# Optimization experiments

Measured on AMD Instinct MI355X. Metric: run time of the kernel, lower is better.

The kernel has to match this reference:

```python
import jax, jax.numpy as jnp
import numpy as np

N = 50000
E = 800000
IN = 128
H = 128
OUT = 64
L = 2
THETA = 1.0
SCALE = 2.0


def setup_inputs() -> dict:
    key = jax.random.key(0)
    ks = jax.random.split(key, 12)
    g = lambda k, s: (jax.random.normal(k, s, jnp.float32) * 0.05)
    return {
        "x": jax.random.normal(ks[0], (N, IN), jnp.float32),
        "edge_index": jax.random.randint(ks[1], (2, E), 0, N),
        "mlp_w1": g(ks[2], (IN, 512)), "mlp_b1": jnp.zeros((512,), jnp.float32),
        "mlp_w2": g(ks[3], (512, 64)), "mlp_b2": jnp.zeros((64,), jnp.float32),
        "mlp_w3": g(ks[4], (64, OUT)), "mlp_b3": jnp.zeros((OUT,), jnp.float32),
        "parsing": jnp.ones((L, OUT, OUT), jnp.float32) / SCALE,
        "lin0_w": g(ks[5], (IN, H)), "lin0_b": jnp.zeros((H,), jnp.float32),
        "lin1_w": g(ks[6], (H, OUT)), "lin1_b": jnp.zeros((OUT,), jnp.float32),
        "conv_w1": g(ks[7], (L, H, H)),
        "conv_w2": g(ks[8], (L, H, H)),
    }


def reference(x, edge_index, mlp_w1, mlp_b1, mlp_w2, mlp_b2, mlp_w3, mlp_b3,
              parsing, lin0_w, lin0_b, lin1_w, lin1_b, conv_w1, conv_w2):
    row, col = edge_index[0], edge_index[1]  # start, end

    # --- learn_soft_edge3 (algebraically exact reduction of outer-product + bmm + diag) ---
    h = jax.nn.relu(x @ mlp_w1 + mlp_b1)
    h = jax.nn.relu(h @ mlp_w2 + mlp_b2)
    logits = h @ mlp_w3 + mlp_b3                      # [N, OUT]
    P = jax.nn.relu(SCALE * parsing[0])               # [OUT, OUT]
    # diag(outer(start,end) @ P)[e,c] = start[e,c] * (end @ P)[e,c]
    ew = jnp.sum(logits[row] * (logits @ P)[col], axis=1)  # [E]
    mean = ew.mean()
    var = jnp.var(ew, ddof=1)                          # torch.var is unbiased
    ew = (ew - mean) * jnp.sqrt(jnp.float32(1e-4) / var) + 1.0

    # --- GCN2 stack ---
    x0 = jax.nn.relu(x @ lin0_w + lin0_b)              # [N, H]
    # gcn_norm with self loops (weight 1)
    loop = jnp.arange(N)
    r = jnp.concatenate([row, loop])
    c = jnp.concatenate([col, loop])
    w = jnp.concatenate([ew, jnp.ones((N,), ew.dtype)])
    deg = jax.ops.segment_sum(w, c, num_segments=N)
    dinv = jnp.where(deg > 0, jax.lax.rsqrt(jnp.where(deg > 0, deg, 1.0)), 0.0)
    norm = dinv[r] * w * dinv[c]                       # [E+N]

    hcur = x0
    alpha = 0.0
    for ln in range(L):
        agg = jax.ops.segment_sum(norm[:, None] * hcur[r], c, num_segments=N)  # [N, H]
        agg = agg * (1.0 - alpha)
        x0a = alpha * x0
        beta = float(np.log(THETA / (ln + 1) + 1.0))
        out = (1.0 - beta) * agg + beta * (agg @ conv_w1[ln]) \
            + (1.0 - beta) * x0a + beta * (x0a @ conv_w2[ln])
        hcur = jax.nn.relu(out)
    return hcur @ lin1_w + lin1_b                      # [N, OUT]
```

## Files before the change

kernel.cpp:

```cpp
#include <hip/hip_runtime.h>
#include <hip/hip_bf16.h>
#include <hip/hip_fp16.h>
#include <math.h>

#define NN 50000
#define NE 800000

typedef __attribute__((ext_vector_type(8))) short bf16x8;
typedef __attribute__((ext_vector_type(4))) float f32x4;

__device__ __forceinline__ short f2bf(float f){
  unsigned u = __float_as_uint(f);
  unsigned r = (u + 0x7fffu + ((u >> 16) & 1u)) >> 16;
  return (short)r;
}
__device__ __forceinline__ float bf2f(short s){
  return __uint_as_float(((unsigned)(unsigned short)s) << 16);
}

__device__ __forceinline__ unsigned f2fp8(float f){
  __half h = __float2half(f * 0.00390625f);
  unsigned hb = (unsigned)__half_as_ushort(h);
  unsigned s = hb >> 15;
  unsigned mag = hb & 0x7fffu;
  mag = mag + 0x3fu + ((mag >> 7) & 1u);
  unsigned m8 = mag >> 7;
  if (m8 > 0x7eu) m8 = 0x7eu;
  return (s << 7) | m8;
}
__device__ __forceinline__ void fp8x4_dec(unsigned u, float2& lo, float2& hi){
  unsigned l = ((u & 0x80u) << 8) | ((u & 0x7fu) << 7)
             | ((u & 0x8000u) << 16) | ((u & 0x7f00u) << 15);
  unsigned h = ((u & 0x800000u) >> 8) | ((u & 0x7f0000u) >> 9)
             | (u & 0x80000000u) | ((u & 0x7f000000u) >> 1);
  __half2 hl = *(__half2*)&l;
  __half2 hh = *(__half2*)&h;
  lo = __half22float2(hl);
  hi = __half22float2(hh);
}
__device__ __forceinline__ float fp8_dot4(unsigned a, unsigned b){
  float2 al, ah, bl, bh;
  fp8x4_dec(a, al, ah); fp8x4_dec(b, bl, bh);
  return al.x*bl.x + al.y*bl.y + ah.x*bh.x + ah.y*bh.y;
}

__global__ __launch_bounds__(256) void prep_k(const float* __restrict__ w1,
    const float* __restrict__ w2, const float* __restrict__ w3, const float* __restrict__ pars,
    const float* __restrict__ lin0w, const float* __restrict__ cw1, const float* __restrict__ lin1w,
    short* __restrict__ w1t, short* __restrict__ w2t, short* __restrict__ w3t, short* __restrict__ Pt,
    short* __restrict__ lin0wt, short* __restrict__ cw1t0, short* __restrict__ cw1t1,
    short* __restrict__ lin1wt, int* __restrict__ cnt, float* __restrict__ scal){
  int idx = blockIdx.x*256 + threadIdx.x;
  if (idx < NN) cnt[idx] = 0;
  if (idx < 16) scal[idx] = 0.0f;
  if (idx < 65536){
    int n = idx >> 7, k = idx & 127;
    w1t[idx] = f2bf(w1[k*512 + n]);
  } else if (idx < 98304){
    int i = idx - 65536; int n = i >> 9, k = i & 511;
    w2t[i] = f2bf(w2[k*64 + n]);
  } else if (idx < 102400){
    int i = idx - 98304; int n = i >> 6, k = i & 63;
    w3t[i] = f2bf(w3[k*64 + n]);
  } else if (idx < 106496){
    int i = idx - 102400; int n = i >> 6, k = i & 63;
    Pt[i] = f2bf(fmaxf(2.f*pars[k*64 + n], 0.f));
  } else if (idx < 122880){
    int i = idx - 106496; int n = i >> 7, k = i & 127;
    lin0wt[i] = f2bf(lin0w[k*128 + n]);
  } else if (idx < 139264){
    int i = idx - 122880; int n = i >> 7, k = i & 127;
    cw1t0[i] = f2bf(cw1[k*128 + n]);
  } else if (idx < 155648){
    int i = idx - 139264; int n = i >> 7, k = i & 127;
    cw1t1[i] = f2bf(cw1[16384 + k*128 + n]);
  } else if (idx < 163840){
    int i = idx - 155648; int n = i >> 7, k = i & 127;
    lin1wt[i] = f2bf(lin1w[k*64 + n]);
  }
}

__global__ __launch_bounds__(256) void mlp_mfma_k(
    const float* __restrict__ x,
    const short* __restrict__ w1t, const float* __restrict__ b1,
    const short* __restrict__ w2t, const float* __restrict__ b2,
    const short* __restrict__ w3t, const float* __restrict__ b3,
    const short* __restrict__ Pt,
    unsigned char* __restrict__ lg8, unsigned char* __restrict__ lgp8,
    short* __restrict__ xb, int M)
{
  __shared__ short xs [32][136];
  __shared__ short h1s[32][264];
  __shared__ short h2s[32][72];
  __shared__ short lgs[32][72];
  const int t = threadIdx.x;
  const int wave = t >> 6, lane = t & 63;
  const int quad = lane >> 4, l16 = lane & 15;
  const int m0 = blockIdx.x * 32;

  for (int task = t; task < 512; task += 256){
    int row = task >> 4, c0 = (task & 15) * 8;
    float4 v0 = make_float4(0,0,0,0), v1 = v0;
    int gm = m0 + row;
    if (gm < M){
      v0 = *(const float4*)(x + (size_t)gm*128 + c0);
      v1 = *(const float4*)(x + (size_t)gm*128 + c0 + 4);
    }
    bf16x8 s;
    s[0]=f2bf(v0.x); s[1]=f2bf(v0.y); s[2]=f2bf(v0.z); s[3]=f2bf(v0.w);
    s[4]=f2bf(v1.x); s[5]=f2bf(v1.y); s[6]=f2bf(v1.z); s[7]=f2bf(v1.w);
    *(bf16x8*)&xs[row][c0] = s;
    if (gm < M) *(bf16x8*)(xb + (size_t)gm*128 + c0) = s;
  }
  __syncthreads();

  f32x4 acc2[2];
  acc2[0] = (f32x4){0.f,0.f,0.f,0.f}; acc2[1] = acc2[0];
  const int n2 = wave*16 + l16;

  #pragma unroll
  for (int half = 0; half < 2; half++){
    {
      f32x4 acc[2][4];
      #pragma unroll
      for (int mt=0;mt<2;mt++)
        #pragma unroll
        for (int nt=0;nt<4;nt++) acc[mt][nt] = (f32x4){0.f,0.f,0.f,0.f};
      #pragma unroll
      for (int k0 = 0; k0 < 128; k0 += 32){
        bf16x8 a0 = *(const bf16x8*)&xs[l16     ][k0 + quad*8];
        bf16x8 a1 = *(const bf16x8*)&xs[16 + l16][k0 + quad*8];
        #pragma unroll
        for (int nt = 0; nt < 4; nt++){
          int n = half*256 + wave*64 + nt*16 + l16;
          bf16x8 b = *(const bf16x8*)(w1t + (size_t)n*128 + k0 + quad*8);
          acc[0][nt] = __builtin_amdgcn_mfma_f32_16x16x32_bf16(a0, b, acc[0][nt], 0,0,0);
          acc[1][nt] = __builtin_amdgcn_mfma_f32_16x16x32_bf16(a1, b, acc[1][nt], 0,0,0);
        }
      }
      #pragma unroll
      for (int nt = 0; nt < 4; nt++){
        int n  = half*256 + wave*64 + nt*16 + l16;
        int cl = wave*64 + nt*16 + l16;
        float bb = b1[n];
        #pragma unroll
        for (int mt = 0; mt < 2; mt++){
          #pragma unroll
          for (int r = 0; r < 4; r++){
            int row = mt*16 + quad*4 + r;
            h1s[row][cl] = f2bf(fmaxf(acc[mt][nt][r] + bb, 0.f));
          }
        }
      }
    }
    __syncthreads();

    for (int k0 = 0; k0 < 256; k0 += 32){
      bf16x8 b  = *(const bf16x8*)(w2t + (size_t)n2*512 + half*256 + k0 + quad*8);
      bf16x8 a0 = *(const bf16x8*)&h1s[l16     ][k0 + quad*8];
      bf16x8 a1 = *(const bf16x8*)&h1s[16 + l16][k0 + quad*8];
      acc2[0] = __builtin_amdgcn_mfma_f32_16x16x32_bf16(a0, b, acc2[0], 0,0,0);
      acc2[1] = __builtin_amdgcn_mfma_f32_16x16x32_bf16(a1, b, acc2[1], 0,0,0);
    }
    if (half == 0) __syncthreads();
  }

  {
    float bb = b2[n2];
    #pragma unroll
    for (int mt = 0; mt < 2; mt++)
      #pragma unroll
      for (int r = 0; r < 4; r++)
        h2s[mt*16 + quad*4 + r][n2] = f2bf(fmaxf(acc2[mt][r] + bb, 0.f));
  }
  __syncthreads();

  {
    f32x4 acc[2];
    acc[0] = (f32x4){0.f,0.f,0.f,0.f}; acc[1] = acc[0];
    for (int k0 = 0; k0 < 64; k0 += 32){
      bf16x8 b  = *(const bf16x8*)(w3t + (size_t)n2*64 + k0 + quad*8);
      bf16x8 a0 = *(const bf16x8*)&h2s[l16     ][k0 + quad*8];
      bf16x8 a1 = *(const bf16x8*)&h2s[16 + l16][k0 + quad*8];
      acc[0] = __builtin_amdgcn_mfma_f32_16x16x32_bf16(a0, b, acc[0], 0,0,0);
      acc[1] = __builtin_amdgcn_mfma_f32_16x16x32_bf16(a1, b, acc[1], 0,0,0);
    }
    float bb = b3[n2];
    #pragma unroll
    for (int mt = 0; mt < 2; mt++)
      #pragma unroll
      for (int r = 0; r < 4; r++)
        lgs[mt*16 + quad*4 + r][n2] = f2bf(acc[mt][r] + bb);
  }
  __syncthreads();

  {
    f32x4 acc[2];
    acc[0] = (f32x4){0.f,0.f,0.f,0.f}; acc[1] = acc[0];
    for (int k0 = 0; k0 < 64; k0 += 32){
      bf16x8 b  = *(const bf16x8*)(Pt + (size_t)n2*64 + k0 + quad*8);
      bf16x8 a0 = *(const bf16x8*)&lgs[l16     ][k0 + quad*8];
      bf16x8 a1 = *(const bf16x8*)&lgs[16 + l16][k0 + quad*8];
      acc[0] = __builtin_amdgcn_mfma_f32_16x16x32_bf16(a0, b, acc[0], 0,0,0);
      acc[1] = __builtin_amdgcn_mfma_f32_16x16x32_bf16(a1, b, acc[1], 0,0,0);
    }
    #pragma unroll
    for (int mt = 0; mt < 2; mt++)
      #pragma unroll
      for (int r = 0; r < 4; r++)
        h2s[mt*16 + quad*4 + r][n2] = f2bf(acc[mt][r]);
  }
  __syncthreads();

  {
    int row = t >> 3, c0 = (t & 7) * 8;
    int gm = m0 + row;
    if (gm < M){
      const short* pl = &lgs[row][c0];
      const short* pp = &h2s[row][c0];
      unsigned a0 = 0, a1 = 0, b0 = 0, b1 = 0;
      #pragma unroll
      for (int j = 0; j < 4; j++){
        a0 |= f2fp8(bf2f(pl[j]))     << (8*j);
        a1 |= f2fp8(bf2f(pl[4+j]))   << (8*j);
        b0 |= f2fp8(bf2f(pp[j]))     << (8*j);
        b1 |= f2fp8(bf2f(pp[4+j]))   << (8*j);
      }
      uint2 av; av.x = a0; av.y = a1;
      uint2 bv; bv.x = b0; bv.y = b1;
      *(uint2*)(lg8  + (size_t)gm*64 + c0) = av;
      *(uint2*)(lgp8 + (size_t)gm*64 + c0) = bv;
    }
  }
}

template<int NT, bool RELU, bool RESID, bool BF16OUT, bool SCALEROW>
__global__ __launch_bounds__(256) void bgemm_k(
    const short* __restrict__ A, const short* __restrict__ Bt,
    const float* __restrict__ bias, const short* __restrict__ extra,
    const float* __restrict__ dinvp,
    float* __restrict__ C, short* __restrict__ Cb, int M, float beta)
{
  const int N = NT*64;
  __shared__ short As[32][136];
  const int t = threadIdx.x;
  const int wave = t >> 6, lane = t & 63;
  const int quad = lane >> 4, l16 = lane & 15;
  const int m0 = blockIdx.x * 32;

  for (int task = t; task < 512; task += 256){
    int row = task >> 4, c0 = (task & 15) * 8;
    bf16x8 v = {0,0,0,0,0,0,0,0};
    if (m0 + row < M) v = *(const bf16x8*)(A + (size_t)(m0+row)*128 + c0);
    *(bf16x8*)&As[row][c0] = v;
  }
  __syncthreads();

  f32x4 acc[2][NT];
  #pragma unroll
  for (int mt=0;mt<2;mt++)
    #pragma unroll
    for (int nt=0;nt<NT;nt++) acc[mt][nt] = (f32x4){0.f,0.f,0.f,0.f};

  #pragma unroll
  for (int k0 = 0; k0 < 128; k0 += 32){
    bf16x8 a0 = *(const bf16x8*)&As[l16     ][k0 + quad*8];
    bf16x8 a1 = *(const bf16x8*)&As[16 + l16][k0 + quad*8];
    #pragma unroll
    for (int nt = 0; nt < NT; nt++){
      int n = (wave*NT + nt)*16 + l16;
      bf16x8 b = *(const bf16x8*)(Bt + (size_t)n*128 + k0 + quad*8);
      acc[0][nt] = __builtin_amdgcn_mfma_f32_16x16x32_bf16(a0, b, acc[0][nt], 0,0,0);
      acc[1][nt] = __builtin_amdgcn_mfma_f32_16x16x32_bf16(a1, b, acc[1][nt], 0,0,0);
    }
  }

  #pragma unroll
  for (int nt = 0; nt < NT; nt++){
    int n = (wave*NT + nt)*16 + l16;
    float bb = (bias != nullptr) ? bias[n] : 0.f;
    #pragma unroll
    for (int mt = 0; mt < 2; mt++){
      #pragma unroll
      for (int r = 0; r < 4; r++){
        int gm = m0 + mt*16 + quad*4 + r;
        if (gm >= M) continue;
        float v = acc[mt][nt][r];
        if (RESID){
          float ex = bf2f(extra[(size_t)gm*N + n]);
          v = beta*v + (1.f - beta)*ex;
        }
        v += bb;
        if (RELU) v = fmaxf(v, 0.f);
        if (SCALEROW) v *= dinvp[gm];
        if (BF16OUT) Cb[(size_t)gm*N + n] = f2bf(v);
        else         C [(size_t)gm*N + n] = v;
      }
    }
  }
}

__global__ __launch_bounds__(256) void count_k(const int* __restrict__ col, int* __restrict__ cnt,
    int* __restrict__ rank, int E){
  int i = (blockIdx.x*256 + threadIdx.x)*4;
  if (i + 3 < E){
    int4 c = *(const int4*)(col + i);
    int r0 = atomicAdd(&cnt[c.x], 1);
    int r1 = atomicAdd(&cnt[c.y], 1);
    int r2 = atomicAdd(&cnt[c.z], 1);
    int r3 = atomicAdd(&cnt[c.w], 1);
    *(int4*)(rank + i) = make_int4(r0, r1, r2, r3);
  } else {
    for (; i < E; i++) rank[i] = atomicAdd(&cnt[col[i]], 1);
  }
}

__global__ __launch_bounds__(256) void scan_sums_k(const int* __restrict__ cnt, int* __restrict__ bsum, int n){
  __shared__ int s[256];
  const int t = threadIdx.x;
  int i = blockIdx.x*1024 + t*4;
  int4 v = make_int4(0,0,0,0);
  if (i + 3 < n) v = *(const int4*)(cnt + i);
  else {
    if (i   < n) v.x = cnt[i];
    if (i+1 < n) v.y = cnt[i+1];
    if (i+2 < n) v.z = cnt[i+2];
    if (i+3 < n) v.w = cnt[i+3];
  }
  s[t] = v.x + v.y + v.z + v.w;
  __syncthreads();
  for (int st = 128; st; st >>= 1){
    if (t < st) s[t] += s[t + st];
    __syncthreads();
  }
  if (t == 0) bsum[blockIdx.x] = s[0];
}

__global__ __launch_bounds__(256) void scan_final_k(const int* __restrict__ cnt, const int* __restrict__ bsum,
    int* __restrict__ off, int n, int total, int nb){
  __shared__ int s[256];
  __shared__ int basebs;
  const int t = threadIdx.x;
  if (t < 64){
    int v = (t < nb && t < (int)blockIdx.x) ? bsum[t] : 0;
    #pragma unroll
    for (int o = 1; o < 64; o <<= 1) v += __shfl_xor(v, o);
    if (t == 0) basebs = v;
  }
  int i = blockIdx.x*1024 + t*4;
  int4 v = make_int4(0,0,0,0);
  if (i + 3 < n) v = *(const int4*)(cnt + i);
  else {
    if (i   < n) v.x = cnt[i];
    if (i+1 < n) v.y = cnt[i+1];
    if (i+2 < n) v.z = cnt[i+2];
    if (i+3 < n) v.w = cnt[i+3];
  }
  int tsum = v.x + v.y + v.z + v.w;
  s[t] = tsum;
  __syncthreads();
  #pragma unroll
  for (int st = 1; st < 256; st <<= 1){
    int a = (t >= st) ? s[t - st] : 0;
    __syncthreads();
    s[t] += a;
    __syncthreads();
  }
  int base = s[t] - tsum + basebs;
  int o0 = base, o1 = o0 + v.x, o2 = o1 + v.y, o3 = o2 + v.z;
  if (i   < n) off[i]   = o0;
  if (i+1 < n) off[i+1] = o1;
  if (i+2 < n) off[i+2] = o2;
  if (i+3 < n) off[i+3] = o3;
  if (blockIdx.x == 0 && t == 0) off[n] = total;
}

__global__ __launch_bounds__(256) void scatter_k(const int* __restrict__ row, const int* __restrict__ col,
    const int* __restrict__ off, const int* __restrict__ rank,
    int2* __restrict__ csr_sd, int E){
  int i = (blockIdx.x*256 + threadIdx.x)*4;
  if (i + 3 < E){
    int4 r = *(const int4*)(row + i);
    int4 c = *(const int4*)(col + i);
    int4 k = *(const int4*)(rank + i);
    int o0 = off[c.x], o1 = off[c.y], o2 = off[c.z], o3 = off[c.w];
    int2 p0; p0.x = r.x; p0.y = c.x;
    int2 p1; p1.x = r.y; p1.y = c.y;
    int2 p2; p2.x = r.z; p2.y = c.z;
    int2 p3; p3.x = r.w; p3.y = c.w;
    csr_sd[o0 + k.x] = p0;
    csr_sd[o1 + k.y] = p1;
    csr_sd[o2 + k.z] = p2;
    csr_sd[o3 + k.w] = p3;
  } else {
    for (; i < E; i++){
      int2 p; p.x = row[i]; p.y = col[i];
      csr_sd[off[col[i]] + rank[i]] = p;
    }
  }
}

__global__ __launch_bounds__(256) void ew2_k(const unsigned char* __restrict__ lg8,
    const unsigned char* __restrict__ lgp8,
    const int2* __restrict__ sd,
    float* __restrict__ w, float* __restrict__ scal, int E){
  const int t = threadIdx.x;
  const int lane = t & 63, wid = t >> 6;
  const int g = lane >> 4, q = lane & 15;
  const int gid = (blockIdx.x*4 + wid)*4 + g;
  const int ngroups = gridDim.x*16;
  float s = 0.f, ss = 0.f;
  for (int base = gid*4; base < E; base += ngroups*4){
    int4 p01 = *(const int4*)(sd + base);
    int4 p23 = *(const int4*)(sd + base + 2);
    unsigned a0 = *(const unsigned*)(lg8  + (size_t)p01.x*64 + q*4);
    unsigned a1 = *(const unsigned*)(lg8  + (size_t)p01.z*64 + q*4);
    unsigned a2 = *(const unsigned*)(lg8  + (size_t)p23.x*64 + q*4);
    unsigned a3 = *(const unsigned*)(lg8  + (size_t)p23.z*64 + q*4);
    unsigned b0 = *(const unsigned*)(lgp8 + (size_t)p01.y*64 + q*4);
    unsigned b1 = *(const unsigned*)(lgp8 + (size_t)p01.w*64 + q*4);
    unsigned b2 = *(const unsigned*)(lgp8 + (size_t)p23.y*64 + q*4);
    unsigned b3 = *(const unsigned*)(lgp8 + (size_t)p23.w*64 + q*4);
    float v0 = fp8_dot4(a0, b0);
    float v1 = fp8_dot4(a1, b1);
    float v2 = fp8_dot4(a2, b2);
    float v3 = fp8_dot4(a3, b3);
    #pragma unroll
    for (int o = 1; o < 16; o <<= 1){
      v0 += __shfl_xor(v0, o); v1 += __shfl_xor(v1, o);
      v2 += __shfl_xor(v2, o); v3 += __shfl_xor(v3, o);
    }
    if (q == 0){
      float4 vv = make_float4(v0*65536.f, v1*65536.f, v2*65536.f, v3*65536.f);
      *(float4*)(w + base) = vv;
      s  += vv.x + vv.y + vv.z + vv.w;
      ss += vv.x*vv.x + vv.y*vv.y + vv.z*vv.z + vv.w*vv.w;
    }
  }
  #pragma unroll
  for (int o = 1; o < 64; o <<= 1){ s += __shfl_xor(s, o); ss += __shfl_xor(ss, o); }
  __shared__ float ls[4], lss[4];
  if (lane == 0){ ls[wid] = s; lss[wid] = ss; }
  __syncthreads();
  if (t == 0){
    atomicAdd(&scal[0], ls[0]+ls[1]+ls[2]+ls[3]);
    atomicAdd(&scal[1], lss[0]+lss[1]+lss[2]+lss[3]);
  }
}

__global__ __launch_bounds__(256) void degnorm_k(float* __restrict__ w, const int* __restrict__ off,
    const float* __restrict__ scal, float* __restrict__ dinv, int Nn, int E){
  int n = blockIdx.x*256 + threadIdx.x;
  if (n < Nn){
    double sum = (double)scal[0], sumsq = (double)scal[1];
    double mean_d = sum / (double)E;
    double var    = (sumsq - sum*sum/(double)E) / (double)(E-1);
    float mean = (float)mean_d;
    float k    = (float)sqrt(1e-4 / var);
    int s = off[n], e = off[n+1];
    float d = 1.0f;
    for (int j = s; j < e; j++){
      float v = (w[j] - mean) * k + 1.0f;
      w[j] = v;
      d += v;
    }
    dinv[n] = (d > 0.f) ? rsqrtf(d) : 0.f;
  }
}

__global__ __launch_bounds__(256) void agg_gather_k(const short* __restrict__ hb,
    const int* __restrict__ off, const int2* __restrict__ sd, const float* __restrict__ w,
    const float* __restrict__ dinv, short* __restrict__ aggb, int Nn){
  int n = blockIdx.x*4 + (threadIdx.x >> 6);
  int lane = threadIdx.x & 63;
  if (n >= Nn) return;
  float d = dinv[n];
  short2 hv = *(const short2*)(hb + (size_t)n*128 + lane*2);
  float acc0 = bf2f(hv.x), acc1 = bf2f(hv.y);
  int s = off[n], e = off[n+1];
  int j = s;
  for (; j + 7 < e; j += 8){
    int4 p0 = *(const int4*)(sd + j);
    int4 p1 = *(const int4*)(sd + j + 2);
    int4 p2 = *(const int4*)(sd + j + 4);
    int4 p3 = *(const int4*)(sd + j + 6);
    float4 w0 = *(const float4*)(w + j);
    float4 w1 = *(const float4*)(w + j + 4);
    short2 h0 = *(const short2*)(hb + (size_t)p0.x*128 + lane*2);
    short2 h1 = *(const short2*)(hb + (size_t)p0.z*128 + lane*2);
    short2 h2 = *(const short2*)(hb + (size_t)p1.x*128 + lane*2);
    short2 h3 = *(const short2*)(hb + (size_t)p1.z*128 + lane*2);
    short2 h4 = *(const short2*)(hb + (size_t)p2.x*128 + lane*2);
    short2 h5 = *(const short2*)(hb + (size_t)p2.z*128 + lane*2);
    short2 h6 = *(const short2*)(hb + (size_t)p3.x*128 + lane*2);
    short2 h7 = *(const short2*)(hb + (size_t)p3.z*128 + lane*2);
    acc0 += w0.x*bf2f(h0.x) + w0.y*bf2f(h1.x) + w0.z*bf2f(h2.x) + w0.w*bf2f(h3.x)
          + w1.x*bf2f(h4.x) + w1.y*bf2f(h5.x) + w1.z*bf2f(h6.x) + w1.w*bf2f(h7.x);
    acc1 += w0.x*bf2f(h0.y) + w0.y*bf2f(h1.y) + w0.z*bf2f(h2.y) + w0.w*bf2f(h3.y)
          + w1.x*bf2f(h4.y) + w1.y*bf2f(h5.y) + w1.z*bf2f(h6.y) + w1.w*bf2f(h7.y);
  }
  for (; j < e; j++){
    int2 p = sd[j];
    short2 h0 = *(const short2*)(hb + (size_t)p.x*128 + lane*2);
    float w0 = w[j];
    acc0 += w0*bf2f(h0.x); acc1 += w0*bf2f(h0.y);
  }
  acc0 *= d; acc1 *= d;
  short2 o; o.x = f2bf(acc0); o.y = f2bf(acc1);
  *(short2*)(aggb + (size_t)n*128 + lane*2) = o;
}

extern "C" void kernel_launch(void* const* d_in, const int* in_sizes, int n_in,
                              void* d_out, int out_size, void* d_ws, size_t ws_size,
                              hipStream_t stream){
  const float* x      = (const float*)d_in[0];
  const int*   ei     = (const int*)  d_in[1];
  const float* w1     = (const float*)d_in[2];
  const float* b1     = (const float*)d_in[3];
  const float* w2     = (const float*)d_in[4];
  const float* b2     = (const float*)d_in[5];
  const float* w3     = (const float*)d_in[6];
  const float* b3     = (const float*)d_in[7];
  const float* pars   = (const float*)d_in[8];
  const float* lin0w  = (const float*)d_in[9];
  const float* lin0b  = (const float*)d_in[10];
  const float* lin1w  = (const float*)d_in[11];
  const float* lin1b  = (const float*)d_in[12];
  const float* cw1    = (const float*)d_in[13];
  float* out          = (float*)d_out;

  float* ws = (float*)d_ws;
  int*   cnt     = (int*)(ws + 0);
  int*   off     = (int*)(ws + 50048);
  int2*  csr_sd  = (int2*)(ws + 150144);
  int*   bsum    = (int*)(ws + 1750400);
  short* lin0wt  = (short*)(ws + 1751000);
  short* cw1t0   = lin0wt + 16384;
  short* cw1t1   = cw1t0 + 16384;
  short* lin1wt  = cw1t1 + 16384;
  unsigned char* lg8  = (unsigned char*)(ws + 1800000);
  unsigned char* lgp8 = (unsigned char*)(ws + 2600000);
  float* csr_w2  = ws + 3400000;
  float* dinv    = ws + 5800000;
  float* scal    = ws + 5850048;
  short* bufAb   = (short*)(ws + 5900000);
  short* bufCb   = (short*)(ws + 9100000);
  short* aggb    = (short*)(ws + 12300000);
  short* bufBb   = (short*)(ws + 15500000);
  short* w1t     = (short*)(ws + 18700000);
  short* w2t     = w1t + 65536;
  short* w3t     = w2t + 32768;
  short* Pt      = w3t + 4096;
  short* xb      = (short*)(ws + 18800000);
  int*   rank    = (int*)(ws + 22000000);

  const int Mn = NN, E = NE;
  const int* erow = ei;
  const int* ecol = ei + E;
  const float beta0 = 0.69314718055994530942f;
  const float beta1 = 0.40546510810816438198f;
  const int nScanB = (Mn + 1023) / 1024;
  const int nGB = (Mn + 31) / 32;
  const int nE4 = (E/4 + 255) / 256;

  prep_k<<<(163840+255)/256, 256, 0, stream>>>(w1, w2, w3, pars, lin0w, cw1, lin1w,
                                               w1t, w2t, w3t, Pt, lin0wt, cw1t0, cw1t1, lin1wt,
                                               cnt, scal);
  count_k<<<nE4, 256, 0, stream>>>(ecol, cnt, rank, E);
  scan_sums_k<<<nScanB, 256, 0, stream>>>(cnt, bsum, Mn);
  scan_final_k<<<nScanB, 256, 0, stream>>>(cnt, bsum, off, Mn, E, nScanB);
  scatter_k<<<nE4, 256, 0, stream>>>(erow, ecol, off, rank, csr_sd, E);
  mlp_mfma_k<<<(Mn+31)/32, 256, 0, stream>>>(x, w1t, b1, w2t, b2, w3t, b3, Pt,
                                             lg8, lgp8, xb, Mn);
  ew2_k<<<1024, 256, 0, stream>>>(lg8, lgp8, csr_sd, csr_w2, scal, E);
  degnorm_k<<<(Mn+255)/256, 256, 0, stream>>>(csr_w2, off, scal, dinv, Mn, E);
  bgemm_k<2,true,false,true,true><<<nGB, 256, 0, stream>>>(xb, lin0wt, lin0b, nullptr, dinv, nullptr, bufAb, Mn, 0.f);
  agg_gather_k<<<(Mn+3)/4, 256, 0, stream>>>(bufAb, off, csr_sd, csr_w2, dinv, aggb, Mn);
  bgemm_k<2,true,true,true,true><<<nGB, 256, 0, stream>>>(aggb, cw1t0, nullptr, aggb, dinv, nullptr, bufCb, Mn, beta0);
  agg_gather_k<<<(Mn+3)/4, 256, 0, stream>>>(bufCb, off, csr_sd, csr_w2, dinv, aggb, Mn);
  bgemm_k<2,true,true,true,false><<<nGB, 256, 0, stream>>>(aggb, cw1t1, nullptr, aggb, nullptr, nullptr, bufBb, Mn, beta1);
  bgemm_k<1,false,false,false,false><<<nGB, 256, 0, stream>>>(bufBb, lin1wt, lin1b, nullptr, nullptr, out, nullptr, Mn, 0.f);
}
```

Baseline: 383.2 us.

## Double MLP kernel row tile to 64 to reuse weight fragments

The fused MLP kernel now handles 64 rows per block instead of 32, so each weight fragment loaded from global memory feeds four MFMA row tiles instead of two. The second layer splits its K loop into two independent accumulator chains to expose more MFMA parallelism, and the fp8 packing epilogue writes 16-byte stores. This cuts redundant weight traffic but doubles LDS use and accumulator registers per block and halves the block count, which may lower occupancy.

```diff
diff --git a/kernel.cpp b/kernel.cpp
--- a/kernel.cpp
+++ b/kernel.cpp
@@ -89,16 +89,16 @@
     unsigned char* __restrict__ lg8, unsigned char* __restrict__ lgp8,
     short* __restrict__ xb, int M)
 {
-  __shared__ short xs [32][136];
-  __shared__ short h1s[32][264];
-  __shared__ short h2s[32][72];
-  __shared__ short lgs[32][72];
+  __shared__ short xs [64][136];
+  __shared__ short h1s[64][264];
+  __shared__ short h2s[64][72];
+  __shared__ short lgs[64][72];
   const int t = threadIdx.x;
   const int wave = t >> 6, lane = t & 63;
   const int quad = lane >> 4, l16 = lane & 15;
-  const int m0 = blockIdx.x * 32;
-
-  for (int task = t; task < 512; task += 256){
+  const int m0 = blockIdx.x * 64;
+
+  for (int task = t; task < 1024; task += 256){
     int row = task >> 4, c0 = (task & 15) * 8;
     float4 v0 = make_float4(0,0,0,0), v1 = v0;
     int gm = m0 + row;
@@ -114,28 +114,33 @@
   }
   __syncthreads();
 
-  f32x4 acc2[2];
-  acc2[0] = (f32x4){0.f,0.f,0.f,0.f}; acc2[1] = acc2[0];
+  f32x4 acc2a[4], acc2b[4];
+  #pragma unroll
+  for (int mt=0;mt<4;mt++){ acc2a[mt] = (f32x4){0.f,0.f,0.f,0.f}; acc2b[mt] = acc2a[mt]; }
   const int n2 = wave*16 + l16;
 
   #pragma unroll
   for (int half = 0; half < 2; half++){
     {
-      f32x4 acc[2][4];
-      #pragma unroll
-      for (int mt=0;mt<2;mt++)
+      f32x4 acc[4][4];
+      #pragma unroll
+      for (int mt=0;mt<4;mt++)
         #pragma unroll
         for (int nt=0;nt<4;nt++) acc[mt][nt] = (f32x4){0.f,0.f,0.f,0.f};
       #pragma unroll
       for (int k0 = 0; k0 < 128; k0 += 32){
         bf16x8 a0 = *(const bf16x8*)&xs[l16     ][k0 + quad*8];
         bf16x8 a1 = *(const bf16x8*)&xs[16 + l16][k0 + quad*8];
+        bf16x8 a2 = *(const bf16x8*)&xs[32 + l16][k0 + quad*8];
+        bf16x8 a3 = *(const bf16x8*)&xs[48 + l16][k0 + quad*8];
         #pragma unroll
         for (int nt = 0; nt < 4; nt++){
           int n = half*256 + wave*64 + nt*16 + l16;
           bf16x8 b = *(const bf16x8*)(w1t + (size_t)n*128 + k0 + quad*8);
           acc[0][nt] = __builtin_amdgcn_mfma_f32_16x16x32_bf16(a0, b, acc[0][nt], 0,0,0);
           acc[1][nt] = __builtin_amdgcn_mfma_f32_16x16x32_bf16(a1, b, acc[1][nt], 0,0,0);
+          acc[2][nt] = __builtin_amdgcn_mfma_f32_16x16x32_bf16(a2, b, acc[2][nt], 0,0,0);
+          acc[3][nt] = __builtin_amdgcn_mfma_f32_16x16x32_bf16(a3, b, acc[3][nt], 0,0,0);
         }
       }
       #pragma unroll
@@ -144,7 +149,7 @@
         int cl = wave*64 + nt*16 + l16;
         float bb = b1[n];
         #pragma unroll
-        for (int mt = 0; mt < 2; mt++){
+        for (int mt = 0; mt < 4; mt++){
           #pragma unroll
           for (int r = 0; r < 4; r++){
             int row = mt*16 + quad*4 + r;
@@ -155,12 +160,17 @@
     }
     __syncthreads();
 
-    for (int k0 = 0; k0 < 256; k0 += 32){
-      bf16x8 b  = *(const bf16x8*)(w2t + (size_t)n2*512 + half*256 + k0 + quad*8);
-      bf16x8 a0 = *(const bf16x8*)&h1s[l16     ][k0 + quad*8];
-      bf16x8 a1 = *(const bf16x8*)&h1s[16 + l16][k0 + quad*8];
-      acc2[0] = __builtin_amdgcn_mfma_f32_16x16x32_bf16(a0, b, acc2[0], 0,0,0);
-      acc2[1] = __builtin_amdgcn_mfma_f32_16x16x32_bf16(a1, b, acc2[1], 0,0,0);
+    #pragma unroll
+    for (int k0 = 0; k0 < 128; k0 += 32){
+      bf16x8 bA = *(const bf16x8*)(w2t + (size_t)n2*512 + half*256 + k0 + quad*8);
+      bf16x8 bB = *(const bf16x8*)(w2t + (size_t)n2*512 + half*256 + 128 + k0 + quad*8);
+      #pragma unroll
+      for (int mt = 0; mt < 4; mt++){
+        bf16x8 aA = *(const bf16x8*)&h1s[mt*16 + l16][k0 + quad*8];
+        bf16x8 aB = *(const bf16x8*)&h1s[mt*16 + l16][128 + k0 + quad*8];
+        acc2a[mt] = __builtin_amdgcn_mfma_f32_16x16x32_bf16(aA, bA, acc2a[mt], 0,0,0);
+        acc2b[mt] = __builtin_amdgcn_mfma_f32_16x16x32_bf16(aB, bB, acc2b[mt], 0,0,0);
+      }
     }
     if (half == 0) __syncthreads();
   }
@@ -168,26 +178,29 @@
   {
     float bb = b2[n2];
     #pragma unroll
-    for (int mt = 0; mt < 2; mt++)
+    for (int mt = 0; mt < 4; mt++)
       #pragma unroll
       for (int r = 0; r < 4; r++)
-        h2s[mt*16 + quad*4 + r][n2] = f2bf(fmaxf(acc2[mt][r] + bb, 0.f));
+        h2s[mt*16 + quad*4 + r][n2] = f2bf(fmaxf(acc2a[mt][r] + acc2b[mt][r] + bb, 0.f));
   }
   __syncthreads();
 
   {
-    f32x4 acc[2];
-    acc[0] = (f32x4){0.f,0.f,0.f,0.f}; acc[1] = acc[0];
+    f32x4 acc[4];
+    #pragma unroll
+    for (int mt=0;mt<4;mt++) acc[mt] = (f32x4){0.f,0.f,0.f,0.f};
+    #pragma unroll
     for (int k0 = 0; k0 < 64; k0 += 32){
-      bf16x8 b  = *(const bf16x8*)(w3t + (size_t)n2*64 + k0 + quad*8);
-      bf16x8 a0 = *(const bf16x8*)&h2s[l16     ][k0 + quad*8];
-      bf16x8 a1 = *(const bf16x8*)&h2s[16 + l16][k0 + quad*8];
-      acc[0] = __builtin_amdgcn_mfma_f32_16x16x32_bf16(a0, b, acc[0], 0,0,0);
-      acc[1] = __builtin_amdgcn_mfma_f32_16x16x32_bf16(a1, b, acc[1], 0,0,0);
+      bf16x8 b = *(const bf16x8*)(w3t + (size_t)n2*64 + k0 + quad*8);
+      #pragma unroll
+      for (int mt = 0; mt < 4; mt++){
+        bf16x8 a = *(const bf16x8*)&h2s[mt*16 + l16][k0 + quad*8];
+        acc[mt] = __builtin_amdgcn_mfma_f32_16x16x32_bf16(a, b, acc[mt], 0,0,0);
+      }
     }
     float bb = b3[n2];
     #pragma unroll
-    for (int mt = 0; mt < 2; mt++)
+    for (int mt = 0; mt < 4; mt++)
       #pragma unroll
       for (int r = 0; r < 4; r++)
         lgs[mt*16 + quad*4 + r][n2] = f2bf(acc[mt][r] + bb);
@@ -195,17 +208,20 @@
   __syncthreads();
 
   {
-    f32x4 acc[2];
-    acc[0] = (f32x4){0.f,0.f,0.f,0.f}; acc[1] = acc[0];
+    f32x4 acc[4];
+    #pragma unroll
+    for (int mt=0;mt<4;mt++) acc[mt] = (f32x4){0.f,0.f,0.f,0.f};
+    #pragma unroll
     for (int k0 = 0; k0 < 64; k0 += 32){
-      bf16x8 b  = *(const bf16x8*)(Pt + (size_t)n2*64 + k0 + quad*8);
-      bf16x8 a0 = *(const bf16x8*)&lgs[l16     ][k0 + quad*8];
-      bf16x8 a1 = *(const bf16x8*)&lgs[16 + l16][k0 + quad*8];
-      acc[0] = __builtin_amdgcn_mfma_f32_16x16x32_bf16(a0, b, acc[0], 0,0,0);
-      acc[1] = __builtin_amdgcn_mfma_f32_16x16x32_bf16(a1, b, acc[1], 0,0,0);
-    }
-    #pragma unroll
-    for (int mt = 0; mt < 2; mt++)
+      bf16x8 b = *(const bf16x8*)(Pt + (size_t)n2*64 + k0 + quad*8);
+      #pragma unroll
+      for (int mt = 0; mt < 4; mt++){
+        bf16x8 a = *(const bf16x8*)&lgs[mt*16 + l16][k0 + quad*8];
+        acc[mt] = __builtin_amdgcn_mfma_f32_16x16x32_bf16(a, b, acc[mt], 0,0,0);
+      }
+    }
+    #pragma unroll
+    for (int mt = 0; mt < 4; mt++)
       #pragma unroll
       for (int r = 0; r < 4; r++)
         h2s[mt*16 + quad*4 + r][n2] = f2bf(acc[mt][r]);
@@ -213,23 +229,24 @@
   __syncthreads();
 
   {
-    int row = t >> 3, c0 = (t & 7) * 8;
+    int row = t >> 2, c0 = (t & 3) * 16;
     int gm = m0 + row;
     if (gm < M){
       const short* pl = &lgs[row][c0];
       const short* pp = &h2s[row][c0];
-      unsigned a0 = 0, a1 = 0, b0 = 0, b1 = 0;
-      #pragma unroll
-      for (int j = 0; j < 4; j++){
-        a0 |= f2fp8(bf2f(pl[j]))     << (8*j);
-        a1 |= f2fp8(bf2f(pl[4+j]))   << (8*j);
-        b0 |= f2fp8(bf2f(pp[j]))     << (8*j);
-        b1 |= f2fp8(bf2f(pp[4+j]))   << (8*j);
+      unsigned a[4] = {0,0,0,0}, b[4] = {0,0,0,0};
+      #pragma unroll
+      for (int q2 = 0; q2 < 4; q2++){
+        #pragma unroll
+        for (int j = 0; j < 4; j++){
+          a[q2] |= f2fp8(bf2f(pl[q2*4+j])) << (8*j);
+          b[q2] |= f2fp8(bf2f(pp[q2*4+j])) << (8*j);
+        }
       }
-      uint2 av; av.x = a0; av.y = a1;
-      uint2 bv; bv.x = b0; bv.y = b1;
-      *(uint2*)(lg8  + (size_t)gm*64 + c0) = av;
-      *(uint2*)(lgp8 + (size_t)gm*64 + c0) = bv;
+      uint4 av; av.x=a[0]; av.y=a[1]; av.z=a[2]; av.w=a[3];
+      uint4 bv; bv.x=b[0]; bv.y=b[1]; bv.z=b[2]; bv.w=b[3];
+      *(uint4*)(lg8  + (size_t)gm*64 + c0) = av;
+      *(uint4*)(lgp8 + (size_t)gm*64 + c0) = bv;
     }
   }
 }
@@ -570,7 +587,7 @@
   scan_sums_k<<<nScanB, 256, 0, stream>>>(cnt, bsum, Mn);
   scan_final_k<<<nScanB, 256, 0, stream>>>(cnt, bsum, off, Mn, E, nScanB);
   scatter_k<<<nE4, 256, 0, stream>>>(erow, ecol, off, rank, csr_sd, E);
-  mlp_mfma_k<<<(Mn+31)/32, 256, 0, stream>>>(x, w1t, b1, w2t, b2, w3t, b3, Pt,
+  mlp_mfma_k<<<(Mn+63)/64, 256, 0, stream>>>(x, w1t, b1, w2t, b2, w3t, b3, Pt,
                                              lg8, lgp8, xb, Mn);
   ew2_k<<<1024, 256, 0, stream>>>(lg8, lgp8, csr_sd, csr_w2, scal, E);
   degnorm_k<<<(Mn+255)/256, 256, 0, stream>>>(csr_w2, off, scal, dinv, Mn, E);
```

Result: faster. 369.8 us (-3.5%).
